# Kernel optimization log

Measured on AMD Instinct MI355X. Metric: run time of the kernel, lower is better.

## Reference

```python
import jax, jax.numpy as jnp
import numpy as np

B, N, IN_F, OUT_F, REL_DIM, NUM_REL = 4, 2048, 256, 128, 10, 6
D = OUT_F // 2  # internal_dim
ALPHA = 0.2
LAMBDA_INIT = 0.8 - 0.6 * float(np.exp(-0.3 * 1))  # depth=1
EPS = 1e-5


def setup_inputs() -> dict:
    key = jax.random.key(0)
    ks = jax.random.split(key, 16)
    return {
        "h": jax.random.normal(ks[0], (B, N, IN_F), jnp.float32),
        "adj": jax.random.randint(ks[1], (B, N, N), 0, NUM_REL, jnp.int32),
        "W": jax.random.normal(ks[2], (IN_F, OUT_F), jnp.float32) * (1.414 / np.sqrt(IN_F)),
        "a_left_pos": jax.random.normal(ks[3], (D,), jnp.float32) * 0.1,
        "a_right_pos": jax.random.normal(ks[4], (D,), jnp.float32) * 0.1,
        "a_left_neg": jax.random.normal(ks[5], (D,), jnp.float32) * 0.1,
        "a_right_neg": jax.random.normal(ks[6], (D,), jnp.float32) * 0.1,
        "rel_emb": jax.random.normal(ks[7], (NUM_REL, REL_DIM), jnp.float32),
        "a_rel_pos": jax.random.normal(ks[8], (REL_DIM,), jnp.float32) * 0.3,
        "a_rel_neg": jax.random.normal(ks[9], (REL_DIM,), jnp.float32) * 0.3,
        "lambda_left1": jax.random.normal(ks[10], (D,), jnp.float32) * 0.1,
        "lambda_right1": jax.random.normal(ks[11], (D,), jnp.float32) * 0.1,
        "lambda_left2": jax.random.normal(ks[12], (D,), jnp.float32) * 0.1,
        "lambda_right2": jax.random.normal(ks[13], (D,), jnp.float32) * 0.1,
        "ln_gamma": jnp.ones((OUT_F,), jnp.float32),
        "ln_beta": jnp.zeros((OUT_F,), jnp.float32),
    }


def _leaky_relu(x):
    return jnp.where(x >= 0, x, ALPHA * x)


def reference(h, adj, W, a_left_pos, a_right_pos, a_left_neg, a_right_neg,
              rel_emb, a_rel_pos, a_rel_neg,
              lambda_left1, lambda_right1, lambda_left2, lambda_right2,
              ln_gamma, ln_beta):
    Wh = jnp.einsum('bnf,fo->bno', h, W)              # [B,N,OUT_F]
    Wh4 = Wh.reshape(B, N, 2, D)
    Wh_pos, Wh_neg = Wh4[:, :, 0, :], Wh4[:, :, 1, :]  # [B,N,D]

    # e[b,i,j] = left[b,i] + right[b,j] + rel_score[adj[b,i,j]]
    # relation Linear(rel_dim,1) applied to embedding rows == per-relation scalar lookup
    rel_score_pos = rel_emb @ a_rel_pos               # [NUM_REL]
    rel_score_neg = rel_emb @ a_rel_neg
    e_pos = (Wh_pos @ a_left_pos)[:, :, None] + (Wh_pos @ a_right_pos)[:, None, :] + rel_score_pos[adj]
    e_neg = (Wh_neg @ a_left_neg)[:, :, None] + (Wh_neg @ a_right_neg)[:, None, :] + rel_score_neg[adj]

    neg_inf = jnp.float32(-9e15)
    mask = adj > 0
    attn_pos = jax.nn.softmax(jnp.where(mask, _leaky_relu(e_pos), neg_inf), axis=2)
    attn_neg = jax.nn.softmax(jnp.where(mask, _leaky_relu(e_neg), neg_inf), axis=2)

    lam1 = jnp.exp(jnp.sum(lambda_left1 * lambda_right1))
    lam2 = jnp.exp(jnp.sum(lambda_left2 * lambda_right2))
    lambda_full = lam1 - lam2 + LAMBDA_INIT
    attention = attn_pos - lambda_full * attn_neg     # [B,N,N]

    Wh_v = jnp.concatenate([Wh_pos, Wh_neg], axis=-1)  # [B,N,OUT_F]
    h_prime = jnp.einsum('bij,bjo->bio', attention, Wh_v)

    mu = jnp.mean(h_prime, axis=-1, keepdims=True)
    var = jnp.mean(jnp.square(h_prime - mu), axis=-1, keepdims=True)
    h_prime = (h_prime - mu) * jax.lax.rsqrt(var + EPS) * ln_gamma + ln_beta
    h_prime = h_prime * (1.0 - LAMBDA_INIT)
    return jax.nn.gelu(h_prime, approximate=False), attention
```

## Files before the change

kernel.cpp:

```cpp
#include <hip/hip_runtime.h>
#include <math.h>

typedef short bf16x8 __attribute__((ext_vector_type(8)));
typedef float f32x4  __attribute__((ext_vector_type(4)));

constexpr int   B_    = 4;
constexpr int   N_    = 2048;
constexpr int   INF_  = 256;
constexpr int   OUTF_ = 128;
constexpr float LAMBDA_INIT_ = 0.35550906759096926f;
constexpr float OUT_SCALE_   = 0.64449093240903074f;
constexpr float EPS_         = 1e-5f;
constexpr float LOG2E_       = 1.44269504088896340736f;

__device__ inline unsigned short f2bf(float x) {
  unsigned u = __float_as_uint(x);
  u += 0x7fffu + ((u >> 16) & 1u);
  return (unsigned short)(u >> 16);
}
__device__ inline unsigned pack2(float a, float b) {
  return (unsigned)f2bf(a) | ((unsigned)f2bf(b) << 16);
}

__global__ void scalars_kernel(const float* __restrict__ rel_emb,
                               const float* __restrict__ a_rel_pos,
                               const float* __restrict__ a_rel_neg,
                               const float* __restrict__ ll1, const float* __restrict__ lr1,
                               const float* __restrict__ ll2, const float* __restrict__ lr2,
                               float* __restrict__ scal) {
  int lane = threadIdx.x;
  float p1 = ll1[lane] * lr1[lane];
  float p2 = ll2[lane] * lr2[lane];
  #pragma unroll
  for (int off = 32; off; off >>= 1) { p1 += __shfl_xor(p1, off); p2 += __shfl_xor(p2, off); }
  if (lane == 0) scal[12] = expf(p1) - expf(p2) + LAMBDA_INIT_;
  if (lane < 6) {
    float sp = 0.f, sn = 0.f;
    for (int k = 0; k < 10; ++k) {
      float rv = rel_emb[lane * 10 + k];
      sp += rv * a_rel_pos[k];
      sn += rv * a_rel_neg[k];
    }
    scal[lane]     = sp * LOG2E_;
    scal[6 + lane] = sn * LOG2E_;
  }
}

__global__ __launch_bounds__(256) void wh_dots_v2(
    const float* __restrict__ h, const float* __restrict__ W,
    const float* __restrict__ alp, const float* __restrict__ arp,
    const float* __restrict__ aln, const float* __restrict__ arn,
    unsigned short* __restrict__ WhvT,
    float* __restrict__ lposv, float* __restrict__ rposv,
    float* __restrict__ lnegv, float* __restrict__ rnegv) {
  __shared__ __align__(16) float hT[32][260];
  const int t = threadIdx.x;
  const int row0 = blockIdx.x * 32;
  const int b = row0 >> 11;

  #pragma unroll 8
  for (int i = 0; i < 32; ++i) hT[i][t] = h[(size_t)(row0 + i) * INF_ + t];
  __syncthreads();

  const int rg = t >> 5;
  const int cg = t & 31;
  const int c0 = cg * 4;
  float acc[4][4] = {{0.f,0.f,0.f,0.f},{0.f,0.f,0.f,0.f},{0.f,0.f,0.f,0.f},{0.f,0.f,0.f,0.f}};

  #pragma unroll 2
  for (int k4 = 0; k4 < 64; ++k4) {
    float4 hv[4], wv[4];
    #pragma unroll
    for (int rr = 0; rr < 4; ++rr)
      hv[rr] = *reinterpret_cast<const float4*>(&hT[rg * 4 + rr][k4 * 4]);
    #pragma unroll
    for (int j = 0; j < 4; ++j)
      wv[j] = *reinterpret_cast<const float4*>(&W[(size_t)(k4 * 4 + j) * OUTF_ + c0]);
    #pragma unroll
    for (int rr = 0; rr < 4; ++rr) {
      const float* hp = reinterpret_cast<const float*>(&hv[rr]);
      #pragma unroll
      for (int j = 0; j < 4; ++j) {
        const float* wp = reinterpret_cast<const float*>(&wv[j]);
        acc[rr][0] += hp[j] * wp[0];
        acc[rr][1] += hp[j] * wp[1];
        acc[rr][2] += hp[j] * wp[2];
        acc[rr][3] += hp[j] * wp[3];
      }
    }
  }

  const int n0 = (row0 & 2047) + rg * 4;
  #pragma unroll
  for (int cc = 0; cc < 4; ++cc) {
    uint2 v;
    v.x = pack2(acc[0][cc], acc[1][cc]);
    v.y = pack2(acc[2][cc], acc[3][cc]);
    *reinterpret_cast<uint2*>(WhvT + ((size_t)b * OUTF_ + c0 + cc) * N_ + n0) = v;
  }

  float aL[4], aR[4];
  #pragma unroll
  for (int cc = 0; cc < 4; ++cc) {
    const int c = c0 + cc;
    aL[cc] = (c < 64) ? alp[c] : aln[c - 64];
    aR[cc] = (c < 64) ? arp[c] : arn[c - 64];
  }
  float sl[4], sr2[4];
  #pragma unroll
  for (int rr = 0; rr < 4; ++rr) {
    sl[rr]  = (acc[rr][0] * aL[0] + acc[rr][1] * aL[1]) + (acc[rr][2] * aL[2] + acc[rr][3] * aL[3]);
    sr2[rr] = (acc[rr][0] * aR[0] + acc[rr][1] * aR[1]) + (acc[rr][2] * aR[2] + acc[rr][3] * aR[3]);
  }
  #pragma unroll
  for (int off = 1; off <= 8; off <<= 1) {
    #pragma unroll
    for (int rr = 0; rr < 4; ++rr) {
      sl[rr]  += __shfl_xor(sl[rr],  off);
      sr2[rr] += __shfl_xor(sr2[rr], off);
    }
  }
  if (cg == 0) {
    #pragma unroll
    for (int rr = 0; rr < 4; ++rr) {
      const int node = row0 + rg * 4 + rr;
      lposv[node] = sl[rr]  * LOG2E_;
      rposv[node] = sr2[rr] * LOG2E_;
    }
  } else if (cg == 16) {
    #pragma unroll
    for (int rr = 0; rr < 4; ++rr) {
      const int node = row0 + rg * 4 + rr;
      lnegv[node] = sl[rr]  * LOG2E_;
      rnegv[node] = sr2[rr] * LOG2E_;
    }
  }
}

__global__ __launch_bounds__(512, 4) void fused_attn_pv(
    const int* __restrict__ adj,
    const float* __restrict__ lposv, const float* __restrict__ rposv,
    const float* __restrict__ lnegv, const float* __restrict__ rnegv,
    const float* __restrict__ scal, const unsigned short* __restrict__ WhvT,
    const float* __restrict__ gamma, const float* __restrict__ beta,
    float* __restrict__ out0, float* __restrict__ out1) {
  __shared__ __align__(16) uint4 A4[16 * 256];
  float* scr = reinterpret_cast<float*>(&A4[15 * 256]);
  float (*hp)[132] = reinterpret_cast<float (*)[132]>(A4);

  const int t = threadIdx.x;
  const int lane = t & 63;
  const int wv = t >> 6;
  const int bi = blockIdx.x;
  const int b  = bi >> 7;
  const int i0 = (bi & 127) * 16;
  const int flat0 = b * N_ + i0;

  const float lam = scal[12];
  float srcP = -1.0e30f, srcN = -1.0e30f;
  if (lane >= 1 && lane <= 5) { srcP = scal[lane]; srcN = scal[6 + lane]; }
  const int iSrcP = __float_as_int(srcP);
  const int iSrcN = __float_as_int(srcN);

  const int j0 = t * 4;
  float4 rp4 = *reinterpret_cast<const float4*>(rposv + b * N_ + j0);
  float4 rn4 = *reinterpret_cast<const float4*>(rnegv + b * N_ + j0);
  const float rp[4] = {rp4.x, rp4.y, rp4.z, rp4.w};
  const float rn[4] = {rn4.x, rn4.y, rn4.z, rn4.w};

  const int wchunk = (t >> 1) >> 5;
  const int wloc   = (t >> 1) & 31;

  int4 avN = *reinterpret_cast<const int4*>(adj + (size_t)flat0 * N_ + j0);

  for (int r = 0; r < 16; ++r) {
    const int flat = flat0 + r;
    const int4 av4 = avN;
    if (r < 15)
      avN = *reinterpret_cast<const int4*>(adj + (size_t)(flat + 1) * N_ + j0);
    const float lP = lposv[flat];
    const float lN = lnegv[flat];
    int av[4] = {av4.x, av4.y, av4.z, av4.w};

    float p[4], n[4];
    #pragma unroll
    for (int q = 0; q < 4; ++q) {
      float rsp = __int_as_float(__builtin_amdgcn_ds_bpermute(av[q] << 2, iSrcP));
      float rsn = __int_as_float(__builtin_amdgcn_ds_bpermute(av[q] << 2, iSrcN));
      float e  = lP + rp[q] + rsp;
      float en = lN + rn[q] + rsn;
      e  = fmaxf(e, 0.2f * e);
      en = fmaxf(en, 0.2f * en);
      p[q] = __builtin_amdgcn_exp2f(e);
      n[q] = __builtin_amdgcn_exp2f(en);
    }
    float sP = (p[0] + p[1]) + (p[2] + p[3]);
    float sN = (n[0] + n[1]) + (n[2] + n[3]);
    #pragma unroll
    for (int off = 32; off; off >>= 1) { sP += __shfl_xor(sP, off); sN += __shfl_xor(sN, off); }
    const int bf = r & 1;
    if (lane == 0) { scr[bf * 16 + wv] = sP; scr[bf * 16 + 8 + wv] = sN; }
    __syncthreads();
    float vP = scr[bf * 16 + (lane & 7)];
    vP += __shfl_xor(vP, 1); vP += __shfl_xor(vP, 2); vP += __shfl_xor(vP, 4);
    float vN = scr[bf * 16 + 8 + (lane & 7)];
    vN += __shfl_xor(vN, 1); vN += __shfl_xor(vN, 2); vN += __shfl_xor(vN, 4);
    const float s1 = 1.f / vP;
    const float s2 = -lam / vN;

    float a[4];
    #pragma unroll
    for (int q = 0; q < 4; ++q) a[q] = p[q] * s1 + n[q] * s2;
    float* o1 = out1 + (size_t)flat * N_ + j0;
    *reinterpret_cast<float4*>(o1) = make_float4(a[0], a[1], a[2], a[3]);

    if (r == 15) __syncthreads();
    const int uidx = r * 256 + wchunk * 32 + (wloc ^ (r & 7));
    uint2 val;
    val.x = pack2(a[0], a[1]); val.y = pack2(a[2], a[3]);
    reinterpret_cast<uint2*>(A4)[uidx * 2 + (t & 1)] = val;
  }
  __syncthreads();

  const int bl  = lane & 15;
  const int kg  = lane >> 4;
  const int ch  = wv * 16 + bl;
  const unsigned short* Bp = WhvT + ((size_t)b * OUTF_ + ch) * N_ + kg * 8;
  f32x4 acc0 = {0.f, 0.f, 0.f, 0.f};
  f32x4 acc1 = {0.f, 0.f, 0.f, 0.f};
  const int arow = bl * 256;
  const int aswz = bl & 7;

  bf16x8 bBuf[2][8];
  #pragma unroll
  for (int kk = 0; kk < 8; ++kk)
    bBuf[0][kk] = *reinterpret_cast<const bf16x8*>(Bp + kk * 32);

  #pragma unroll
  for (int c = 0; c < 8; ++c) {
    const int cur = c & 1;
    if (c < 7) {
      #pragma unroll
      for (int kk = 0; kk < 8; ++kk)
        bBuf[cur ^ 1][kk] = *reinterpret_cast<const bf16x8*>(Bp + (c + 1) * 256 + kk * 32);
    }
    #pragma unroll
    for (int kk = 0; kk < 8; ++kk) {
      bf16x8 a = *reinterpret_cast<const bf16x8*>(&A4[arow + c * 32 + ((kk * 4 + kg) ^ aswz)]);
      if (cur == 0) acc0 = __builtin_amdgcn_mfma_f32_16x16x32_bf16(a, bBuf[0][kk], acc0, 0, 0, 0);
      else          acc1 = __builtin_amdgcn_mfma_f32_16x16x32_bf16(a, bBuf[1][kk], acc1, 0, 0, 0);
    }
  }
  __syncthreads();

  #pragma unroll
  for (int q = 0; q < 4; ++q) hp[kg * 4 + q][ch] = acc0[q] + acc1[q];
  __syncthreads();

  const int row = t >> 5;
  const int c0  = t & 31;
  float v[4], s = 0.f, sq = 0.f;
  #pragma unroll
  for (int e = 0; e < 4; ++e) {
    v[e] = hp[row][c0 + e * 32];
    s += v[e]; sq += v[e] * v[e];
  }
  #pragma unroll
  for (int off = 16; off; off >>= 1) { s += __shfl_xor(s, off); sq += __shfl_xor(sq, off); }
  const float mu  = s  * (1.f / 128.f);
  const float var = sq * (1.f / 128.f) - mu * mu;
  const float inv = rsqrtf(var + EPS_);
  float* orow = out0 + ((size_t)(b * N_ + i0 + row)) * OUTF_;
  #pragma unroll
  for (int e = 0; e < 4; ++e) {
    const int chh = c0 + e * 32;
    float y = (v[e] - mu) * inv * gamma[chh] + beta[chh];
    y *= OUT_SCALE_;
    orow[chh] = 0.5f * y * (1.f + erff(y * 0.70710678118654752f));
  }
}

extern "C" void kernel_launch(void* const* d_in, const int* in_sizes, int n_in,
                              void* d_out, int out_size, void* d_ws, size_t ws_size,
                              hipStream_t stream) {
  (void)in_sizes; (void)n_in; (void)out_size; (void)ws_size;
  const float* h        = (const float*)d_in[0];
  const int*   adj      = (const int*)d_in[1];
  const float* W        = (const float*)d_in[2];
  const float* alp      = (const float*)d_in[3];
  const float* arp      = (const float*)d_in[4];
  const float* aln      = (const float*)d_in[5];
  const float* arn      = (const float*)d_in[6];
  const float* rel_emb  = (const float*)d_in[7];
  const float* a_rel_p  = (const float*)d_in[8];
  const float* a_rel_n  = (const float*)d_in[9];
  const float* ll1      = (const float*)d_in[10];
  const float* lr1      = (const float*)d_in[11];
  const float* ll2      = (const float*)d_in[12];
  const float* lr2      = (const float*)d_in[13];
  const float* gamma    = (const float*)d_in[14];
  const float* beta     = (const float*)d_in[15];

  float* out0 = (float*)d_out;
  float* out1 = out0 + (size_t)B_ * N_ * OUTF_;

  float* ws    = (float*)d_ws;
  float* scal  = ws;
  float* lposv = ws + 32;
  float* rposv = lposv + B_ * N_;
  float* lnegv = rposv + B_ * N_;
  float* rnegv = lnegv + B_ * N_;
  unsigned short* WhvT = (unsigned short*)(rnegv + B_ * N_);

  scalars_kernel<<<1, 64, 0, stream>>>(rel_emb, a_rel_p, a_rel_n, ll1, lr1, ll2, lr2, scal);
  wh_dots_v2<<<(B_ * N_) / 32, 256, 0, stream>>>(h, W, alp, arp, aln, arn,
                                                 WhvT, lposv, rposv, lnegv, rnegv);
  fused_attn_pv<<<B_ * (N_ / 16), 512, 0, stream>>>(adj, lposv, rposv, lnegv, rnegv,
                                                    scal, WhvT, gamma, beta, out0, out1);
}
```

Before: 81.97 us.

## Assign whole attention rows per wavefront to remove per-row block barriers

The softmax phase is reorganised so each wavefront owns two full rows, keeping 32 p/n values per lane in registers. Row sums then reduce within the wavefront, which removes the shared-memory scratch and one block-wide barrier per row. The cost is higher register pressure, no overlap of the next row's adj load with current compute (all 8 chunks are loaded per row instead), and repeated loads of rposv/rnegv per row.

```diff
diff --git a/kernel.cpp b/kernel.cpp
--- a/kernel.cpp
+++ b/kernel.cpp
@@ -145,7 +145,6 @@
     const float* __restrict__ gamma, const float* __restrict__ beta,
     float* __restrict__ out0, float* __restrict__ out1) {
   __shared__ __align__(16) uint4 A4[16 * 256];
-  float* scr = reinterpret_cast<float*>(&A4[15 * 256]);
   float (*hp)[132] = reinterpret_cast<float (*)[132]>(A4);
 
   const int t = threadIdx.x;
@@ -162,63 +161,57 @@
   const int iSrcP = __float_as_int(srcP);
   const int iSrcN = __float_as_int(srcN);
 
-  const int j0 = t * 4;
-  float4 rp4 = *reinterpret_cast<const float4*>(rposv + b * N_ + j0);
-  float4 rn4 = *reinterpret_cast<const float4*>(rnegv + b * N_ + j0);
-  const float rp[4] = {rp4.x, rp4.y, rp4.z, rp4.w};
-  const float rn[4] = {rn4.x, rn4.y, rn4.z, rn4.w};
-
-  const int wchunk = (t >> 1) >> 5;
-  const int wloc   = (t >> 1) & 31;
-
-  int4 avN = *reinterpret_cast<const int4*>(adj + (size_t)flat0 * N_ + j0);
-
-  for (int r = 0; r < 16; ++r) {
-    const int flat = flat0 + r;
-    const int4 av4 = avN;
-    if (r < 15)
-      avN = *reinterpret_cast<const int4*>(adj + (size_t)(flat + 1) * N_ + j0);
+  #pragma unroll
+  for (int rr = 0; rr < 2; ++rr) {
+    const int row = wv * 2 + rr;
+    const int flat = flat0 + row;
     const float lP = lposv[flat];
     const float lN = lnegv[flat];
-    int av[4] = {av4.x, av4.y, av4.z, av4.w};
-
-    float p[4], n[4];
-    #pragma unroll
-    for (int q = 0; q < 4; ++q) {
-      float rsp = __int_as_float(__builtin_amdgcn_ds_bpermute(av[q] << 2, iSrcP));
-      float rsn = __int_as_float(__builtin_amdgcn_ds_bpermute(av[q] << 2, iSrcN));
-      float e  = lP + rp[q] + rsp;
-      float en = lN + rn[q] + rsn;
-      e  = fmaxf(e, 0.2f * e);
-      en = fmaxf(en, 0.2f * en);
-      p[q] = __builtin_amdgcn_exp2f(e);
-      n[q] = __builtin_amdgcn_exp2f(en);
-    }
-    float sP = (p[0] + p[1]) + (p[2] + p[3]);
-    float sN = (n[0] + n[1]) + (n[2] + n[3]);
+
+    float p[8][4], n[8][4];
+    float sP = 0.f, sN = 0.f;
+    #pragma unroll
+    for (int c2 = 0; c2 < 8; ++c2) {
+      const int j = c2 * 256 + lane * 4;
+      int4   av4 = *reinterpret_cast<const int4*>(adj + (size_t)flat * N_ + j);
+      float4 rp4 = *reinterpret_cast<const float4*>(rposv + b * N_ + j);
+      float4 rn4 = *reinterpret_cast<const float4*>(rnegv + b * N_ + j);
+      int   av[4] = {av4.x, av4.y, av4.z, av4.w};
+      float rpv[4] = {rp4.x, rp4.y, rp4.z, rp4.w};
+      float rnv[4] = {rn4.x, rn4.y, rn4.z, rn4.w};
+      #pragma unroll
+      for (int q = 0; q < 4; ++q) {
+        float rsp = __int_as_float(__builtin_amdgcn_ds_bpermute(av[q] << 2, iSrcP));
+        float rsn = __int_as_float(__builtin_amdgcn_ds_bpermute(av[q] << 2, iSrcN));
+        float e  = lP + rpv[q] + rsp;
+        float en = lN + rnv[q] + rsn;
+        e  = fmaxf(e, 0.2f * e);
+        en = fmaxf(en, 0.2f * en);
+        p[c2][q] = __builtin_amdgcn_exp2f(e);
+        n[c2][q] = __builtin_amdgcn_exp2f(en);
+        sP += p[c2][q];
+        sN += n[c2][q];
+      }
+    }
     #pragma unroll
     for (int off = 32; off; off >>= 1) { sP += __shfl_xor(sP, off); sN += __shfl_xor(sN, off); }
-    const int bf = r & 1;
-    if (lane == 0) { scr[bf * 16 + wv] = sP; scr[bf * 16 + 8 + wv] = sN; }
-    __syncthreads();
-    float vP = scr[bf * 16 + (lane & 7)];
-    vP += __shfl_xor(vP, 1); vP += __shfl_xor(vP, 2); vP += __shfl_xor(vP, 4);
-    float vN = scr[bf * 16 + 8 + (lane & 7)];
-    vN += __shfl_xor(vN, 1); vN += __shfl_xor(vN, 2); vN += __shfl_xor(vN, 4);
-    const float s1 = 1.f / vP;
-    const float s2 = -lam / vN;
-
-    float a[4];
-    #pragma unroll
-    for (int q = 0; q < 4; ++q) a[q] = p[q] * s1 + n[q] * s2;
-    float* o1 = out1 + (size_t)flat * N_ + j0;
-    *reinterpret_cast<float4*>(o1) = make_float4(a[0], a[1], a[2], a[3]);
-
-    if (r == 15) __syncthreads();
-    const int uidx = r * 256 + wchunk * 32 + (wloc ^ (r & 7));
-    uint2 val;
-    val.x = pack2(a[0], a[1]); val.y = pack2(a[2], a[3]);
-    reinterpret_cast<uint2*>(A4)[uidx * 2 + (t & 1)] = val;
+    const float s1 = 1.f / sP;
+    const float s2 = -lam / sN;
+
+    const int swz = row & 7;
+    float* o1 = out1 + (size_t)flat * N_;
+    #pragma unroll
+    for (int c2 = 0; c2 < 8; ++c2) {
+      float a0 = p[c2][0] * s1 + n[c2][0] * s2;
+      float a1 = p[c2][1] * s1 + n[c2][1] * s2;
+      float a2 = p[c2][2] * s1 + n[c2][2] * s2;
+      float a3 = p[c2][3] * s1 + n[c2][3] * s2;
+      *reinterpret_cast<float4*>(o1 + c2 * 256 + lane * 4) = make_float4(a0, a1, a2, a3);
+      const int uidx = row * 256 + c2 * 32 + ((lane >> 1) ^ swz);
+      uint2 val;
+      val.x = pack2(a0, a1); val.y = pack2(a2, a3);
+      reinterpret_cast<uint2*>(A4)[uidx * 2 + (lane & 1)] = val;
+    }
   }
   __syncthreads();
 
```

After: 111.4 us. 1.36x slower.

## Precompute softmax row sums in a pre-pass and fold scalars kernel into wh_dots

Applied to the files above, without the earlier changes.

The tiny scalars kernel is merged into block 0 of the Wh projection kernel, which removes one launch. In the attention kernel, each wave first computes the positive and negative exp-sums for two rows by reading the adj rows directly. The main 16-row loop then drops its per-row cross-wave reduction and __syncthreads. The cost is reading adj twice and doing the exp work twice per element, in exchange for fewer block-wide barriers per row.

```diff
diff --git a/kernel.cpp b/kernel.cpp
--- a/kernel.cpp
+++ b/kernel.cpp
@@ -22,41 +22,41 @@
   return (unsigned)f2bf(a) | ((unsigned)f2bf(b) << 16);
 }
 
-__global__ void scalars_kernel(const float* __restrict__ rel_emb,
-                               const float* __restrict__ a_rel_pos,
-                               const float* __restrict__ a_rel_neg,
-                               const float* __restrict__ ll1, const float* __restrict__ lr1,
-                               const float* __restrict__ ll2, const float* __restrict__ lr2,
-                               float* __restrict__ scal) {
-  int lane = threadIdx.x;
-  float p1 = ll1[lane] * lr1[lane];
-  float p2 = ll2[lane] * lr2[lane];
-  #pragma unroll
-  for (int off = 32; off; off >>= 1) { p1 += __shfl_xor(p1, off); p2 += __shfl_xor(p2, off); }
-  if (lane == 0) scal[12] = expf(p1) - expf(p2) + LAMBDA_INIT_;
-  if (lane < 6) {
-    float sp = 0.f, sn = 0.f;
-    for (int k = 0; k < 10; ++k) {
-      float rv = rel_emb[lane * 10 + k];
-      sp += rv * a_rel_pos[k];
-      sn += rv * a_rel_neg[k];
-    }
-    scal[lane]     = sp * LOG2E_;
-    scal[6 + lane] = sn * LOG2E_;
-  }
-}
-
-__global__ __launch_bounds__(256) void wh_dots_v2(
+__global__ __launch_bounds__(256) void wh_dots_v3(
     const float* __restrict__ h, const float* __restrict__ W,
     const float* __restrict__ alp, const float* __restrict__ arp,
     const float* __restrict__ aln, const float* __restrict__ arn,
+    const float* __restrict__ rel_emb,
+    const float* __restrict__ a_rel_pos, const float* __restrict__ a_rel_neg,
+    const float* __restrict__ ll1, const float* __restrict__ lr1,
+    const float* __restrict__ ll2, const float* __restrict__ lr2,
     unsigned short* __restrict__ WhvT,
     float* __restrict__ lposv, float* __restrict__ rposv,
-    float* __restrict__ lnegv, float* __restrict__ rnegv) {
+    float* __restrict__ lnegv, float* __restrict__ rnegv,
+    float* __restrict__ scal) {
   __shared__ __align__(16) float hT[32][260];
   const int t = threadIdx.x;
   const int row0 = blockIdx.x * 32;
   const int b = row0 >> 11;
+
+  if (blockIdx.x == 0 && t < 64) {
+    const int lane = t;
+    float p1 = ll1[lane] * lr1[lane];
+    float p2 = ll2[lane] * lr2[lane];
+    #pragma unroll
+    for (int off = 32; off; off >>= 1) { p1 += __shfl_xor(p1, off); p2 += __shfl_xor(p2, off); }
+    if (lane == 0) scal[12] = expf(p1) - expf(p2) + LAMBDA_INIT_;
+    if (lane < 6) {
+      float sp = 0.f, sn = 0.f;
+      for (int k = 0; k < 10; ++k) {
+        float rv = rel_emb[lane * 10 + k];
+        sp += rv * a_rel_pos[k];
+        sn += rv * a_rel_neg[k];
+      }
+      scal[lane]     = sp * LOG2E_;
+      scal[6 + lane] = sn * LOG2E_;
+    }
+  }
 
   #pragma unroll 8
   for (int i = 0; i < 32; ++i) hT[i][t] = h[(size_t)(row0 + i) * INF_ + t];
@@ -137,7 +137,7 @@
   }
 }
 
-__global__ __launch_bounds__(512, 4) void fused_attn_pv(
+__global__ __launch_bounds__(512, 4) void fused_attn_pv2(
     const int* __restrict__ adj,
     const float* __restrict__ lposv, const float* __restrict__ rposv,
     const float* __restrict__ lnegv, const float* __restrict__ rnegv,
@@ -145,7 +145,7 @@
     const float* __restrict__ gamma, const float* __restrict__ beta,
     float* __restrict__ out0, float* __restrict__ out1) {
   __shared__ __align__(16) uint4 A4[16 * 256];
-  float* scr = reinterpret_cast<float*>(&A4[15 * 256]);
+  __shared__ float scr[32];
   float (*hp)[132] = reinterpret_cast<float (*)[132]>(A4);
 
   const int t = threadIdx.x;
@@ -162,6 +162,40 @@
   const int iSrcP = __float_as_int(srcP);
   const int iSrcN = __float_as_int(srcN);
 
+  #pragma unroll
+  for (int rr = 0; rr < 2; ++rr) {
+    const int row = wv * 2 + rr;
+    const int flat = flat0 + row;
+    const float lP = lposv[flat];
+    const float lN = lnegv[flat];
+    float sP = 0.f, sN = 0.f;
+    #pragma unroll
+    for (int c2 = 0; c2 < 8; ++c2) {
+      const int j = c2 * 256 + lane * 4;
+      int4   av4 = *reinterpret_cast<const int4*>(adj + (size_t)flat * N_ + j);
+      float4 rp4 = *reinterpret_cast<const float4*>(rposv + b * N_ + j);
+      float4 rn4 = *reinterpret_cast<const float4*>(rnegv + b * N_ + j);
+      int   av[4] = {av4.x, av4.y, av4.z, av4.w};
+      float rpv[4] = {rp4.x, rp4.y, rp4.z, rp4.w};
+      float rnv[4] = {rn4.x, rn4.y, rn4.z, rn4.w};
+      #pragma unroll
+      for (int q = 0; q < 4; ++q) {
+        float rsp = __int_as_float(__builtin_amdgcn_ds_bpermute(av[q] << 2, iSrcP));
+        float rsn = __int_as_float(__builtin_amdgcn_ds_bpermute(av[q] << 2, iSrcN));
+        float e  = lP + rpv[q] + rsp;
+        float en = lN + rnv[q] + rsn;
+        e  = fmaxf(e, 0.2f * e);
+        en = fmaxf(en, 0.2f * en);
+        sP += __builtin_amdgcn_exp2f(e);
+        sN += __builtin_amdgcn_exp2f(en);
+      }
+    }
+    #pragma unroll
+    for (int off = 32; off; off >>= 1) { sP += __shfl_xor(sP, off); sN += __shfl_xor(sN, off); }
+    if (lane == 0) { scr[row] = sP; scr[16 + row] = sN; }
+  }
+  __syncthreads();
+
   const int j0 = t * 4;
   float4 rp4 = *reinterpret_cast<const float4*>(rposv + b * N_ + j0);
   float4 rn4 = *reinterpret_cast<const float4*>(rnegv + b * N_ + j0);
@@ -173,6 +207,7 @@
 
   int4 avN = *reinterpret_cast<const int4*>(adj + (size_t)flat0 * N_ + j0);
 
+  #pragma unroll 4
   for (int r = 0; r < 16; ++r) {
     const int flat = flat0 + r;
     const int4 av4 = avN;
@@ -194,19 +229,8 @@
       p[q] = __builtin_amdgcn_exp2f(e);
       n[q] = __builtin_amdgcn_exp2f(en);
     }
-    float sP = (p[0] + p[1]) + (p[2] + p[3]);
-    float sN = (n[0] + n[1]) + (n[2] + n[3]);
-    #pragma unroll
-    for (int off = 32; off; off >>= 1) { sP += __shfl_xor(sP, off); sN += __shfl_xor(sN, off); }
-    const int bf = r & 1;
-    if (lane == 0) { scr[bf * 16 + wv] = sP; scr[bf * 16 + 8 + wv] = sN; }
-    __syncthreads();
-    float vP = scr[bf * 16 + (lane & 7)];
-    vP += __shfl_xor(vP, 1); vP += __shfl_xor(vP, 2); vP += __shfl_xor(vP, 4);
-    float vN = scr[bf * 16 + 8 + (lane & 7)];
-    vN += __shfl_xor(vN, 1); vN += __shfl_xor(vN, 2); vN += __shfl_xor(vN, 4);
-    const float s1 = 1.f / vP;
-    const float s2 = -lam / vN;
+    const float s1 = 1.f / scr[r];
+    const float s2 = -lam / scr[16 + r];
 
     float a[4];
     #pragma unroll
@@ -214,7 +238,6 @@
     float* o1 = out1 + (size_t)flat * N_ + j0;
     *reinterpret_cast<float4*>(o1) = make_float4(a[0], a[1], a[2], a[3]);
 
-    if (r == 15) __syncthreads();
     const int uidx = r * 256 + wchunk * 32 + (wloc ^ (r & 7));
     uint2 val;
     val.x = pack2(a[0], a[1]); val.y = pack2(a[2], a[3]);
@@ -312,9 +335,10 @@
   float* rnegv = lnegv + B_ * N_;
   unsigned short* WhvT = (unsigned short*)(rnegv + B_ * N_);
 
-  scalars_kernel<<<1, 64, 0, stream>>>(rel_emb, a_rel_p, a_rel_n, ll1, lr1, ll2, lr2, scal);
-  wh_dots_v2<<<(B_ * N_) / 32, 256, 0, stream>>>(h, W, alp, arp, aln, arn,
-                                                 WhvT, lposv, rposv, lnegv, rnegv);
-  fused_attn_pv<<<B_ * (N_ / 16), 512, 0, stream>>>(adj, lposv, rposv, lnegv, rnegv,
-                                                    scal, WhvT, gamma, beta, out0, out1);
-}
+  wh_dots_v3<<<(B_ * N_) / 32, 256, 0, stream>>>(h, W, alp, arp, aln, arn,
+                                                 rel_emb, a_rel_p, a_rel_n,
+                                                 ll1, lr1, ll2, lr2,
+                                                 WhvT, lposv, rposv, lnegv, rnegv, scal);
+  fused_attn_pv2<<<B_ * (N_ / 16), 512, 0, stream>>>(adj, lposv, rposv, lnegv, rnegv,
+                                                     scal, WhvT, gamma, beta, out0, out1);
+}
```

Measured after the change: 79.37 us, median of 2. 3.2% less time.
